# Performance work log

Hardware: AMD Instinct MI355X
Metric: run time of the kernel (lower is better)

Reference implementation:

```python
import jax, jax.numpy as jnp
import numpy as np

B, S, F, H, L = 4096, 512, 8, 10, 2


def setup_inputs() -> dict:
    key = jax.random.key(0)
    ks = jax.random.split(key, 12)
    bound = 1.0 / np.sqrt(H)  # PyTorch LSTM/Linear init scale
    u = lambda k, shape: jax.random.uniform(k, shape, jnp.float32, -bound, bound)
    return {
        "input_tensor": jax.random.normal(ks[0], (B, S, F), jnp.float32),
        "hidden": jnp.zeros((L, B, H), jnp.float32),
        "cell": jnp.zeros((L, B, H), jnp.float32),
        # layer 0 (input size F), layer 1 (input size H); gate order i,f,g,o
        "W_ih0": u(ks[1], (4 * H, F)), "W_hh0": u(ks[2], (4 * H, H)),
        "b_ih0": u(ks[3], (4 * H,)),   "b_hh0": u(ks[4], (4 * H,)),
        "W_ih1": u(ks[5], (4 * H, H)), "W_hh1": u(ks[6], (4 * H, H)),
        "b_ih1": u(ks[7], (4 * H,)),   "b_hh1": u(ks[8], (4 * H,)),
        "W_fc": u(ks[9], (1, H)),      "b_fc": u(ks[10], (1,)),
    }


def _lstm_layer(x_sbf, h0, c0, W_ih, W_hh, b_ih, b_hh):
    # x_sbf: [S, B, Fin]; h0,c0: [B, H]. Returns hs [S,B,H], (hT, cT).
    b = b_ih + b_hh

    def step(carry, x):
        h, c = carry
        gates = x @ W_ih.T + h @ W_hh.T + b  # [B, 4H]
        i, f, g, o = jnp.split(gates, 4, axis=-1)
        c = jax.nn.sigmoid(f) * c + jax.nn.sigmoid(i) * jnp.tanh(g)
        h = jax.nn.sigmoid(o) * jnp.tanh(c)
        return (h, c), h

    (hT, cT), hs = jax.lax.scan(step, (h0, c0), x_sbf)
    return hs, hT, cT


def reference(input_tensor, hidden, cell,
              W_ih0, W_hh0, b_ih0, b_hh0,
              W_ih1, W_hh1, b_ih1, b_hh1,
              W_fc, b_fc):
    x = jnp.transpose(input_tensor, (1, 0, 2))  # [S, B, F]
    hs0, h0T, c0T = _lstm_layer(x, hidden[0], cell[0], W_ih0, W_hh0, b_ih0, b_hh0)
    hs1, h1T, c1T = _lstm_layer(hs0, hidden[1], cell[1], W_ih1, W_hh1, b_ih1, b_hh1)
    out = hs1[-1]                      # last timestep, [B, H]
    out_regression = out @ W_fc.T + b_fc  # [B, 1]
    hidden_out = jnp.stack([h0T, h1T])
    cell_out = jnp.stack([c0T, c1T])
    return out_regression, hidden_out, cell_out
```

## Files before the change

### kernel.cpp

```cpp
#include <hip/hip_runtime.h>


typedef __fp16 v2h __attribute__((ext_vector_type(2)));
typedef __fp16 v8h __attribute__((ext_vector_type(8)));
struct h4 { v2h a, b, c, d; };

#define L2E 1.4426950408889634f

__device__ __forceinline__ v2h pkh(float a, float b) {
    return __builtin_amdgcn_cvt_pkrtz(a, b);
}
__device__ __forceinline__ float bpermf(int baddr, float v) {
    int r = __builtin_amdgcn_ds_bpermute(baddr, __builtin_bit_cast(int, v));
    return __builtin_bit_cast(float, r);
}

#define SIGM(a)  __builtin_amdgcn_rcpf(1.0f + __builtin_amdgcn_exp2f(-(a)))
#define TANHP(a) fmaf(-2.0f, __builtin_amdgcn_rcpf(1.0f + __builtin_amdgcn_exp2f(a)), 1.0f)
#define DOT2(acc, w, v) (acc) = __builtin_amdgcn_fdot2((w), (v), (acc), false)

__global__ __launch_bounds__(256, 2)
void lstm2_r10(const float* __restrict__ x,
               const float* __restrict__ hid,
               const float* __restrict__ cel,
               const float* __restrict__ Wih0, const float* __restrict__ Whh0,
               const float* __restrict__ bih0, const float* __restrict__ bhh0,
               const float* __restrict__ Wih1, const float* __restrict__ Whh1,
               const float* __restrict__ bih1, const float* __restrict__ bhh1,
               const float* __restrict__ Wfc,  const float* __restrict__ bfc,
               float* __restrict__ out)
{
    __shared__ __attribute__((aligned(16))) __fp16 h0buf[16][6][24];
    __shared__ __attribute__((aligned(16))) __fp16 h1buf[6][24];
    __shared__ float fcb[6][10];

    const int tid  = threadIdx.x;
    const int lane = tid & 63;
    const int wid  = tid >> 6;
    const int uwid = __builtin_amdgcn_readfirstlane(wid);
    int grp = lane / 20;
    int l20 = lane - grp * 20;
    if (lane >= 60) { grp = 2; l20 = 19; }
    const int  ju       = (l20 < 10) ? l20 : l20 - 10;
    const bool unitlane = (l20 < 10);
    const int  eIw = (wid & 1) * 3 + grp;
    const int  e   = blockIdx.x * 6 + eIw;
    const int  ec  = (e < 4095) ? e : 4095;
    const int  baddr = ((l20 < 10) ? (lane + 10) : lane) * 4;

    const float alpha2 = unitlane ? 2.0f : 1.0f;
    const float beta2  = unitlane ? -1.0f : 0.0f;
    const float scB    = unitlane ? 2.0f * L2E : L2E;
    const int   rA = l20, rB = 20 + l20;

#define READROW(PTR, H)                                                      \
    { v8h w0_ = *(const v8h*)(PTR);                                          \
      v2h w1_ = *(const v2h*)((PTR) + 8);                                    \
      h4 q_ = __builtin_bit_cast(h4, w0_);                                   \
      H[0]=q_.a; H[1]=q_.b; H[2]=q_.c; H[3]=q_.d; H[4]=w1_; }

    if (uwid < 2) {
        v2h wxA[4], wxB[4], whA[5], whB[5];
        #pragma unroll
        for (int k = 0; k < 4; ++k) {
            wxA[k] = pkh(Wih0[rA*8+2*k]*L2E, Wih0[rA*8+2*k+1]*L2E);
            wxB[k] = pkh(Wih0[rB*8+2*k]*scB, Wih0[rB*8+2*k+1]*scB);
        }
        #pragma unroll
        for (int k = 0; k < 5; ++k) {
            whA[k] = pkh(Whh0[rA*10+2*k]*L2E, Whh0[rA*10+2*k+1]*L2E);
            whB[k] = pkh(Whh0[rB*10+2*k]*scB, Whh0[rB*10+2*k+1]*scB);
        }
        const float bA = (bih0[rA] + bhh0[rA]) * L2E;
        const float bB = (bih0[rB] + bhh0[rB]) * scB;

        v2h hv[5];
        #pragma unroll
        for (int k = 0; k < 5; ++k) hv[k] = pkh(hid[ec*10+2*k], hid[ec*10+2*k+1]);
        float cc = cel[ec * 10 + ju];
        float hj = 0.0f;

        __fp16* const wbase = &h0buf[0][eIw][0];
        __fp16* const wlane = wbase + l20;

        const float4* __restrict__ xp = reinterpret_cast<const float4*>(x + (size_t)ec * 4096);
        float4 xb0[2], xb1[2], xb2[2], xb3[2];
        xb0[0]=xp[0]; xb0[1]=xp[1];  xb1[0]=xp[2]; xb1[1]=xp[3];
        xb2[0]=xp[4]; xb2[1]=xp[5];  xb3[0]=xp[6]; xb3[1]=xp[7];

        float axA[2], axB[2];
        {
            v2h x0=pkh(xb0[0].x,xb0[0].y), x1=pkh(xb0[0].z,xb0[0].w);
            v2h x2=pkh(xb0[1].x,xb0[1].y), x3=pkh(xb0[1].z,xb0[1].w);
            xb0[0]=xp[8]; xb0[1]=xp[9];
            float nA=bA, nB=bB;
            DOT2(nA,wxA[0],x0); DOT2(nB,wxB[0],x0);
            DOT2(nA,wxA[1],x1); DOT2(nB,wxB[1],x1);
            DOT2(nA,wxA[2],x2); DOT2(nB,wxB[2],x2);
            DOT2(nA,wxA[3],x3); DOT2(nB,wxB[3],x3);
            axA[0]=nA; axB[0]=nB;
        }

#define L0STEP(S, XB, TN, PC, PN)                                            \
        {                                                                    \
            v2h x0=pkh(XB[0].x,XB[0].y), x1=pkh(XB[0].z,XB[0].w);            \
            v2h x2=pkh(XB[1].x,XB[1].y), x3=pkh(XB[1].z,XB[1].w);            \
            { int tn=(TN)>511?511:(TN); XB[0]=xp[2*tn]; XB[1]=xp[2*tn+1]; }  \
            float nA=bA, nB=bB;                                              \
            DOT2(nA,wxA[0],x0); DOT2(nB,wxB[0],x0);                          \
            DOT2(nA,wxA[1],x1); DOT2(nB,wxB[1],x1);                          \
            DOT2(nA,wxA[2],x2); DOT2(nB,wxB[2],x2);                          \
            DOT2(nA,wxA[3],x3); DOT2(nB,wxB[3],x3);                          \
            axA[PN]=nA; axB[PN]=nB;                                          \
            float aA=axA[PC], aB=axB[PC];                                    \
            DOT2(aA,whA[0],hv[0]); DOT2(aB,whB[0],hv[0]);                    \
            DOT2(aA,whA[1],hv[1]); DOT2(aB,whB[1],hv[1]);                    \
            DOT2(aA,whA[2],hv[2]); DOT2(aB,whB[2],hv[2]);                    \
            DOT2(aA,whA[3],hv[3]); DOT2(aB,whB[3],hv[3]);                    \
            DOT2(aA,whA[4],hv[4]); DOT2(aB,whB[4],hv[4]);                    \
            float r1 = SIGM(aA);                                             \
            float r2 = __builtin_amdgcn_rcpf(1.0f + __builtin_amdgcn_exp2f(-aB)); \
            float act2 = fmaf(alpha2, r2, beta2);                            \
            float ig = r1 * act2;                                            \
            float sf = bpermf(baddr, r1);                                    \
            float so = bpermf(baddr, act2);                                  \
            cc = fmaf(sf, cc, ig);                                           \
            hj = so * TANHP((2.0f*L2E) * cc);                                \
            wlane[(S)*144] = (__fp16)hj;                                     \
            READROW(wbase + (S)*144, hv)                                     \
        }

        for (int it = 0; it < 32; ++it) {
            const int tb = 16 * it;
            L0STEP(0,  xb1, tb+5,  0, 1)
            L0STEP(1,  xb2, tb+6,  1, 0)
            L0STEP(2,  xb3, tb+7,  0, 1)
            L0STEP(3,  xb0, tb+8,  1, 0)
            L0STEP(4,  xb1, tb+9,  0, 1)
            L0STEP(5,  xb2, tb+10, 1, 0)
            L0STEP(6,  xb3, tb+11, 0, 1)
            L0STEP(7,  xb0, tb+12, 1, 0)
            __syncthreads();
            L0STEP(8,  xb1, tb+13, 0, 1)
            L0STEP(9,  xb2, tb+14, 1, 0)
            L0STEP(10, xb3, tb+15, 0, 1)
            L0STEP(11, xb0, tb+16, 1, 0)
            L0STEP(12, xb1, tb+17, 0, 1)
            L0STEP(13, xb2, tb+18, 1, 0)
            L0STEP(14, xb3, tb+19, 0, 1)
            L0STEP(15, xb0, tb+20, 1, 0)
            __syncthreads();
        }
#undef L0STEP

        __syncthreads();
        if (unitlane && e < 4096) {
            out[4096          + e * 10 + ju] = hj;
            out[4096 + 81920  + e * 10 + ju] = cc;
        }

    } else {
        v2h wiA[5], wiB[5], whA[5], whB[5];
        #pragma unroll
        for (int k = 0; k < 5; ++k) {
            wiA[k] = pkh(Wih1[rA*10+2*k]*L2E, Wih1[rA*10+2*k+1]*L2E);
            wiB[k] = pkh(Wih1[rB*10+2*k]*scB, Wih1[rB*10+2*k+1]*scB);
            whA[k] = pkh(Whh1[rA*10+2*k]*L2E, Whh1[rA*10+2*k+1]*L2E);
            whB[k] = pkh(Whh1[rB*10+2*k]*scB, Whh1[rB*10+2*k+1]*scB);
        }
        const float bA = (bih1[rA] + bhh1[rA]) * L2E;
        const float bB = (bih1[rB] + bhh1[rB]) * scB;
        const float wfc = Wfc[ju];

        v2h hv[5];
        #pragma unroll
        for (int k = 0; k < 5; ++k) hv[k] = pkh(hid[40960+ec*10+2*k], hid[40960+ec*10+2*k+1]);
        float cc = cel[40960 + ec * 10 + ju];
        float hj = 0.0f;

        const __fp16* const rbase = &h0buf[0][eIw][0];
        __fp16* const h1w  = &h1buf[eIw][0];
        __fp16* const h1wl = h1w + l20;

        float axA[2], axB[2];

#define L1PRE(S, P)                                                          \
        {                                                                    \
            v2h pr[5];                                                       \
            READROW(rbase + (S)*144, pr)                                     \
            float nA=bA, nB=bB;                                              \
            DOT2(nA,wiA[0],pr[0]); DOT2(nB,wiB[0],pr[0]);                    \
            DOT2(nA,wiA[1],pr[1]); DOT2(nB,wiB[1],pr[1]);                    \
            DOT2(nA,wiA[2],pr[2]); DOT2(nB,wiB[2],pr[2]);                    \
            DOT2(nA,wiA[3],pr[3]); DOT2(nB,wiB[3],pr[3]);                    \
            DOT2(nA,wiA[4],pr[4]); DOT2(nB,wiB[4],pr[4]);                    \
            axA[P]=nA; axB[P]=nB;                                            \
        }

#define L1CORE(PC)                                                           \
        {                                                                    \
            float aA=axA[PC], aB=axB[PC];                                    \
            DOT2(aA,whA[0],hv[0]); DOT2(aB,whB[0],hv[0]);                    \
            DOT2(aA,whA[1],hv[1]); DOT2(aB,whB[1],hv[1]);                    \
            DOT2(aA,whA[2],hv[2]); DOT2(aB,whB[2],hv[2]);                    \
            DOT2(aA,whA[3],hv[3]); DOT2(aB,whB[3],hv[3]);                    \
            DOT2(aA,whA[4],hv[4]); DOT2(aB,whB[4],hv[4]);                    \
            float r1 = SIGM(aA);                                             \
            float r2 = __builtin_amdgcn_rcpf(1.0f + __builtin_amdgcn_exp2f(-aB)); \
            float act2 = fmaf(alpha2, r2, beta2);                            \
            float ig = r1 * act2;                                            \
            float sf = bpermf(baddr, r1);                                    \
            float so = bpermf(baddr, act2);                                  \
            cc = fmaf(sf, cc, ig);                                           \
            hj = so * TANHP((2.0f*L2E) * cc);                                \
            h1wl[0] = (__fp16)hj;                                            \
            READROW(h1w, hv)                                                 \
        }

        for (int it = 0; it < 32; ++it) {
            __syncthreads();
            L1PRE(0, 0)
            L1PRE(1, 1) L1CORE(0)
            L1PRE(2, 0) L1CORE(1)
            L1PRE(3, 1) L1CORE(0)
            L1PRE(4, 0) L1CORE(1)
            L1PRE(5, 1) L1CORE(0)
            L1PRE(6, 0) L1CORE(1)
            L1PRE(7, 1) L1CORE(0)
            L1CORE(1)
            __syncthreads();
            L1PRE(8, 0)
            L1PRE(9,  1) L1CORE(0)
            L1PRE(10, 0) L1CORE(1)
            L1PRE(11, 1) L1CORE(0)
            L1PRE(12, 0) L1CORE(1)
            L1PRE(13, 1) L1CORE(0)
            L1PRE(14, 0) L1CORE(1)
            L1PRE(15, 1) L1CORE(0)
            L1CORE(1)
        }
#undef L1PRE
#undef L1CORE

        if (unitlane) fcb[eIw][ju] = hj * wfc;
        __syncthreads();
        if (l20 == 0 && e < 4096) {
            float p = bfc[0];
            #pragma unroll
            for (int k = 0; k < 10; ++k) p += fcb[eIw][k];
            out[e] = p;
        }
        if (unitlane && e < 4096) {
            out[4096 + 40960  + e * 10 + ju] = hj;
            out[4096 + 122880 + e * 10 + ju] = cc;
        }
    }
}

extern "C" void kernel_launch(void* const* d_in, const int* in_sizes, int n_in,
                              void* d_out, int out_size, void* d_ws, size_t ws_size,
                              hipStream_t stream) {
    const float* x    = (const float*)d_in[0];
    const float* hid  = (const float*)d_in[1];
    const float* cel  = (const float*)d_in[2];
    const float* Wih0 = (const float*)d_in[3];
    const float* Whh0 = (const float*)d_in[4];
    const float* bih0 = (const float*)d_in[5];
    const float* bhh0 = (const float*)d_in[6];
    const float* Wih1 = (const float*)d_in[7];
    const float* Whh1 = (const float*)d_in[8];
    const float* bih1 = (const float*)d_in[9];
    const float* bhh1 = (const float*)d_in[10];
    const float* Wfc  = (const float*)d_in[11];
    const float* bfc  = (const float*)d_in[12];

    hipLaunchKernelGGL(lstm2_r10, dim3(683), dim3(256), 0, stream,
                       x, hid, cel, Wih0, Whh0, bih0, bhh0,
                       Wih1, Whh1, bih1, bhh1, Wfc, bfc,
                       (float*)d_out);
}
```

Baseline: 160.5 us.

## Double h0 ring to 32 slots and software-pipeline layer-1 LDS reads

Grows the layer-0 hidden-state ring buffer shared with the layer-1 waves from 16 to 32 timesteps, which halves the number of block barriers per sequence. The x prefetch now uses a pointer advanced per iteration with constant offsets and a peeled last iteration, replacing the clamped index arithmetic. Layer 1 issues the LDS read for step t+2 before the input dot products and recurrent core of earlier steps, hiding LDS latency behind compute. The larger LDS footprint and the extra live registers may affect occupancy.

```diff
diff --git a/kernel.cpp b/kernel.cpp
--- a/kernel.cpp
+++ b/kernel.cpp
@@ -19,8 +19,14 @@
 #define TANHP(a) fmaf(-2.0f, __builtin_amdgcn_rcpf(1.0f + __builtin_amdgcn_exp2f(a)), 1.0f)
 #define DOT2(acc, w, v) (acc) = __builtin_amdgcn_fdot2((w), (v), (acc), false)
 
+#define READROW(PTR, H)                                                      \
+    { v8h w0_ = *(const v8h*)(PTR);                                          \
+      v2h w1_ = *(const v2h*)((PTR) + 8);                                    \
+      h4 q_ = __builtin_bit_cast(h4, w0_);                                   \
+      H[0]=q_.a; H[1]=q_.b; H[2]=q_.c; H[3]=q_.d; H[4]=w1_; }
+
 __global__ __launch_bounds__(256, 2)
-void lstm2_r10(const float* __restrict__ x,
+void lstm2_r17(const float* __restrict__ x,
                const float* __restrict__ hid,
                const float* __restrict__ cel,
                const float* __restrict__ Wih0, const float* __restrict__ Whh0,
@@ -30,20 +36,19 @@
                const float* __restrict__ Wfc,  const float* __restrict__ bfc,
                float* __restrict__ out)
 {
-    __shared__ __attribute__((aligned(16))) __fp16 h0buf[16][6][24];
+    __shared__ __attribute__((aligned(16))) __fp16 h0buf[32][6][24];
     __shared__ __attribute__((aligned(16))) __fp16 h1buf[6][24];
     __shared__ float fcb[6][10];
 
     const int tid  = threadIdx.x;
     const int lane = tid & 63;
-    const int wid  = tid >> 6;
-    const int uwid = __builtin_amdgcn_readfirstlane(wid);
+    const int uwid = __builtin_amdgcn_readfirstlane(tid >> 6);
     int grp = lane / 20;
     int l20 = lane - grp * 20;
     if (lane >= 60) { grp = 2; l20 = 19; }
     const int  ju       = (l20 < 10) ? l20 : l20 - 10;
     const bool unitlane = (l20 < 10);
-    const int  eIw = (wid & 1) * 3 + grp;
+    const int  eIw = (uwid & 1) * 3 + grp;
     const int  e   = blockIdx.x * 6 + eIw;
     const int  ec  = (e < 4095) ? e : 4095;
     const int  baddr = ((l20 < 10) ? (lane + 10) : lane) * 4;
@@ -53,12 +58,6 @@
     const float scB    = unitlane ? 2.0f * L2E : L2E;
     const int   rA = l20, rB = 20 + l20;
 
-#define READROW(PTR, H)                                                      \
-    { v8h w0_ = *(const v8h*)(PTR);                                          \
-      v2h w1_ = *(const v2h*)((PTR) + 8);                                    \
-      h4 q_ = __builtin_bit_cast(h4, w0_);                                   \
-      H[0]=q_.a; H[1]=q_.b; H[2]=q_.c; H[3]=q_.d; H[4]=w1_; }
-
     if (uwid < 2) {
         v2h wxA[4], wxB[4], whA[5], whB[5];
         #pragma unroll
@@ -83,16 +82,16 @@
         __fp16* const wbase = &h0buf[0][eIw][0];
         __fp16* const wlane = wbase + l20;
 
-        const float4* __restrict__ xp = reinterpret_cast<const float4*>(x + (size_t)ec * 4096);
+        const float4* __restrict__ xp4 = reinterpret_cast<const float4*>(x + (size_t)ec * 4096);
         float4 xb0[2], xb1[2], xb2[2], xb3[2];
-        xb0[0]=xp[0]; xb0[1]=xp[1];  xb1[0]=xp[2]; xb1[1]=xp[3];
-        xb2[0]=xp[4]; xb2[1]=xp[5];  xb3[0]=xp[6]; xb3[1]=xp[7];
+        xb0[0]=xp4[0]; xb0[1]=xp4[1];  xb1[0]=xp4[2]; xb1[1]=xp4[3];
+        xb2[0]=xp4[4]; xb2[1]=xp4[5];  xb3[0]=xp4[6]; xb3[1]=xp4[7];
 
         float axA[2], axB[2];
         {
             v2h x0=pkh(xb0[0].x,xb0[0].y), x1=pkh(xb0[0].z,xb0[0].w);
             v2h x2=pkh(xb0[1].x,xb0[1].y), x3=pkh(xb0[1].z,xb0[1].w);
-            xb0[0]=xp[8]; xb0[1]=xp[9];
+            xb0[0]=xp4[8]; xb0[1]=xp4[9];
             float nA=bA, nB=bB;
             DOT2(nA,wxA[0],x0); DOT2(nB,wxB[0],x0);
             DOT2(nA,wxA[1],x1); DOT2(nB,wxB[1],x1);
@@ -101,11 +100,11 @@
             axA[0]=nA; axB[0]=nB;
         }
 
-#define L0STEP(S, XB, TN, PC, PN)                                            \
+#define L0STEP(S, XB, DOREF, PC, PN)                                         \
         {                                                                    \
             v2h x0=pkh(XB[0].x,XB[0].y), x1=pkh(XB[0].z,XB[0].w);            \
             v2h x2=pkh(XB[1].x,XB[1].y), x3=pkh(XB[1].z,XB[1].w);            \
-            { int tn=(TN)>511?511:(TN); XB[0]=xp[2*tn]; XB[1]=xp[2*tn+1]; }  \
+            if (DOREF) { XB[0]=xr[2*((S)+5)]; XB[1]=xr[2*((S)+5)+1]; }       \
             float nA=bA, nB=bB;                                              \
             DOT2(nA,wxA[0],x0); DOT2(nB,wxB[0],x0);                          \
             DOT2(nA,wxA[1],x1); DOT2(nB,wxB[1],x1);                          \
@@ -130,28 +129,44 @@
             READROW(wbase + (S)*144, hv)                                     \
         }
 
-        for (int it = 0; it < 32; ++it) {
-            const int tb = 16 * it;
-            L0STEP(0,  xb1, tb+5,  0, 1)
-            L0STEP(1,  xb2, tb+6,  1, 0)
-            L0STEP(2,  xb3, tb+7,  0, 1)
-            L0STEP(3,  xb0, tb+8,  1, 0)
-            L0STEP(4,  xb1, tb+9,  0, 1)
-            L0STEP(5,  xb2, tb+10, 1, 0)
-            L0STEP(6,  xb3, tb+11, 0, 1)
-            L0STEP(7,  xb0, tb+12, 1, 0)
+#define L0HALF1(RF)                                                          \
+            L0STEP(0,  xb1, 1,  0, 1)  L0STEP(1,  xb2, 1,  1, 0)             \
+            L0STEP(2,  xb3, 1,  0, 1)  L0STEP(3,  xb0, 1,  1, 0)             \
+            L0STEP(4,  xb1, 1,  0, 1)  L0STEP(5,  xb2, 1,  1, 0)             \
+            L0STEP(6,  xb3, 1,  0, 1)  L0STEP(7,  xb0, 1,  1, 0)             \
+            L0STEP(8,  xb1, 1,  0, 1)  L0STEP(9,  xb2, 1,  1, 0)             \
+            L0STEP(10, xb3, 1,  0, 1)  L0STEP(11, xb0, 1,  1, 0)             \
+            L0STEP(12, xb1, 1,  0, 1)  L0STEP(13, xb2, 1,  1, 0)             \
+            L0STEP(14, xb3, 1,  0, 1)  L0STEP(15, xb0, RF, 1, 0)
+
+        const float4* __restrict__ xr = xp4;
+        for (int it = 0; it < 15; ++it) {
+            L0HALF1(1)
             __syncthreads();
-            L0STEP(8,  xb1, tb+13, 0, 1)
-            L0STEP(9,  xb2, tb+14, 1, 0)
-            L0STEP(10, xb3, tb+15, 0, 1)
-            L0STEP(11, xb0, tb+16, 1, 0)
-            L0STEP(12, xb1, tb+17, 0, 1)
-            L0STEP(13, xb2, tb+18, 1, 0)
-            L0STEP(14, xb3, tb+19, 0, 1)
-            L0STEP(15, xb0, tb+20, 1, 0)
+            L0STEP(16, xb1, 1, 0, 1)  L0STEP(17, xb2, 1, 1, 0)
+            L0STEP(18, xb3, 1, 0, 1)  L0STEP(19, xb0, 1, 1, 0)
+            L0STEP(20, xb1, 1, 0, 1)  L0STEP(21, xb2, 1, 1, 0)
+            L0STEP(22, xb3, 1, 0, 1)  L0STEP(23, xb0, 1, 1, 0)
+            L0STEP(24, xb1, 1, 0, 1)  L0STEP(25, xb2, 1, 1, 0)
+            L0STEP(26, xb3, 1, 0, 1)  L0STEP(27, xb0, 1, 1, 0)
+            L0STEP(28, xb1, 1, 0, 1)  L0STEP(29, xb2, 1, 1, 0)
+            L0STEP(30, xb3, 1, 0, 1)  L0STEP(31, xb0, 1, 1, 0)
             __syncthreads();
-        }
+            xr += 64;
+        }
+        L0HALF1(1)
+        __syncthreads();
+        L0STEP(16, xb1, 1, 0, 1)  L0STEP(17, xb2, 1, 1, 0)
+        L0STEP(18, xb3, 1, 0, 1)  L0STEP(19, xb0, 1, 1, 0)
+        L0STEP(20, xb1, 1, 0, 1)  L0STEP(21, xb2, 1, 1, 0)
+        L0STEP(22, xb3, 1, 0, 1)  L0STEP(23, xb0, 1, 1, 0)
+        L0STEP(24, xb1, 1, 0, 1)  L0STEP(25, xb2, 1, 1, 0)
+        L0STEP(26, xb3, 1, 0, 1)  L0STEP(27, xb0, 0, 1, 0)
+        L0STEP(28, xb1, 0, 0, 1)  L0STEP(29, xb2, 0, 1, 0)
+        L0STEP(30, xb3, 0, 0, 1)  L0STEP(31, xb0, 0, 1, 0)
+        __syncthreads();
 #undef L0STEP
+#undef L0HALF1
 
         __syncthreads();
         if (unitlane && e < 4096) {
@@ -182,24 +197,23 @@
         __fp16* const h1w  = &h1buf[eIw][0];
         __fp16* const h1wl = h1w + l20;
 
-        float axA[2], axB[2];
-
-#define L1PRE(S, P)                                                          \
+        v2h prA[5], prB[5];
+        float ax0A, ax0B, ax1A, ax1B;
+
+#define L1RD(PR, S)  READROW(rbase + (S)*144, PR)
+#define L1DOTS(PR, AXA, AXB)                                                 \
         {                                                                    \
-            v2h pr[5];                                                       \
-            READROW(rbase + (S)*144, pr)                                     \
             float nA=bA, nB=bB;                                              \
-            DOT2(nA,wiA[0],pr[0]); DOT2(nB,wiB[0],pr[0]);                    \
-            DOT2(nA,wiA[1],pr[1]); DOT2(nB,wiB[1],pr[1]);                    \
-            DOT2(nA,wiA[2],pr[2]); DOT2(nB,wiB[2],pr[2]);                    \
-            DOT2(nA,wiA[3],pr[3]); DOT2(nB,wiB[3],pr[3]);                    \
-            DOT2(nA,wiA[4],pr[4]); DOT2(nB,wiB[4],pr[4]);                    \
-            axA[P]=nA; axB[P]=nB;                                            \
-        }
-
-#define L1CORE(PC)                                                           \
+            DOT2(nA,wiA[0],PR[0]); DOT2(nB,wiB[0],PR[0]);                    \
+            DOT2(nA,wiA[1],PR[1]); DOT2(nB,wiB[1],PR[1]);                    \
+            DOT2(nA,wiA[2],PR[2]); DOT2(nB,wiB[2],PR[2]);                    \
+            DOT2(nA,wiA[3],PR[3]); DOT2(nB,wiB[3],PR[3]);                    \
+            DOT2(nA,wiA[4],PR[4]); DOT2(nB,wiB[4],PR[4]);                    \
+            AXA=nA; AXB=nB;                                                  \
+        }
+#define L1CORE(AXA, AXB)                                                     \
         {                                                                    \
-            float aA=axA[PC], aB=axB[PC];                                    \
+            float aA=AXA, aB=AXB;                                            \
             DOT2(aA,whA[0],hv[0]); DOT2(aB,whB[0],hv[0]);                    \
             DOT2(aA,whA[1],hv[1]); DOT2(aB,whB[1],hv[1]);                    \
             DOT2(aA,whA[2],hv[2]); DOT2(aB,whB[2],hv[2]);                    \
@@ -217,29 +231,35 @@
             READROW(h1w, hv)                                                 \
         }
 
-        for (int it = 0; it < 32; ++it) {
+#define L1HALF(W)                                                            \
+        L1RD(prA, (W)+0)                                                     \
+        L1RD(prB, (W)+1)  L1DOTS(prA, ax0A, ax0B)                            \
+        L1RD(prA, (W)+2)  L1DOTS(prB, ax1A, ax1B)  L1CORE(ax0A, ax0B)        \
+        L1RD(prB, (W)+3)  L1DOTS(prA, ax0A, ax0B)  L1CORE(ax1A, ax1B)        \
+        L1RD(prA, (W)+4)  L1DOTS(prB, ax1A, ax1B)  L1CORE(ax0A, ax0B)        \
+        L1RD(prB, (W)+5)  L1DOTS(prA, ax0A, ax0B)  L1CORE(ax1A, ax1B)        \
+        L1RD(prA, (W)+6)  L1DOTS(prB, ax1A, ax1B)  L1CORE(ax0A, ax0B)        \
+        L1RD(prB, (W)+7)  L1DOTS(prA, ax0A, ax0B)  L1CORE(ax1A, ax1B)        \
+        L1RD(prA, (W)+8)  L1DOTS(prB, ax1A, ax1B)  L1CORE(ax0A, ax0B)        \
+        L1RD(prB, (W)+9)  L1DOTS(prA, ax0A, ax0B)  L1CORE(ax1A, ax1B)        \
+        L1RD(prA, (W)+10) L1DOTS(prB, ax1A, ax1B)  L1CORE(ax0A, ax0B)        \
+        L1RD(prB, (W)+11) L1DOTS(prA, ax0A, ax0B)  L1CORE(ax1A, ax1B)        \
+        L1RD(prA, (W)+12) L1DOTS(prB, ax1A, ax1B)  L1CORE(ax0A, ax0B)        \
+        L1RD(prB, (W)+13) L1DOTS(prA, ax0A, ax0B)  L1CORE(ax1A, ax1B)        \
+        L1RD(prA, (W)+14) L1DOTS(prB, ax1A, ax1B)  L1CORE(ax0A, ax0B)        \
+        L1RD(prB, (W)+15) L1DOTS(prA, ax0A, ax0B)  L1CORE(ax1A, ax1B)        \
+                          L1DOTS(prB, ax1A, ax1B)  L1CORE(ax0A, ax0B)        \
+                                                   L1CORE(ax1A, ax1B)
+
+        for (int it = 0; it < 16; ++it) {
             __syncthreads();
-            L1PRE(0, 0)
-            L1PRE(1, 1) L1CORE(0)
-            L1PRE(2, 0) L1CORE(1)
-            L1PRE(3, 1) L1CORE(0)
-            L1PRE(4, 0) L1CORE(1)
-            L1PRE(5, 1) L1CORE(0)
-            L1PRE(6, 0) L1CORE(1)
-            L1PRE(7, 1) L1CORE(0)
-            L1CORE(1)
+            L1HALF(0)
             __syncthreads();
-            L1PRE(8, 0)
-            L1PRE(9,  1) L1CORE(0)
-            L1PRE(10, 0) L1CORE(1)
-            L1PRE(11, 1) L1CORE(0)
-            L1PRE(12, 0) L1CORE(1)
-            L1PRE(13, 1) L1CORE(0)
-            L1PRE(14, 0) L1CORE(1)
-            L1PRE(15, 1) L1CORE(0)
-            L1CORE(1)
-        }
-#undef L1PRE
+            L1HALF(16)
+        }
+#undef L1HALF
+#undef L1RD
+#undef L1DOTS
 #undef L1CORE
 
         if (unitlane) fcb[eIw][ju] = hj * wfc;
@@ -274,7 +294,7 @@
     const float* Wfc  = (const float*)d_in[11];
     const float* bfc  = (const float*)d_in[12];
 
-    hipLaunchKernelGGL(lstm2_r10, dim3(683), dim3(256), 0, stream,
+    hipLaunchKernelGGL(lstm2_r17, dim3(683), dim3(256), 0, stream,
                        x, hid, cel, Wih0, Whh0, bih0, bhh0,
                        Wih1, Whh1, bih1, bhh1, Wfc, bfc,
                        (float*)d_out);
```

Result: no change. 159.6 us (-0.6%).
